# Kernel tuning notes

Measured on AMD Instinct MI355X. Metric: run time of the kernel, lower is better.

Reference implementation:

```python
import jax, jax.numpy as jnp
import numpy as np

NEG_SLOPE = 0.2

def setup_inputs() -> dict:
    key = jax.random.key(0)
    k1, k2, k3, k4 = jax.random.split(key, 4)
    B, n, d_in, d_out = 8, 2048, 128, 128
    x = jax.random.normal(k1, (B, n, d_in), dtype=jnp.float32)
    adj = jax.random.uniform(k2, (B, n, n), dtype=jnp.float32)
    # glorot init for W: std = sqrt(2/(fan_in+fan_out))
    W = jax.random.normal(k3, (d_in, d_out), dtype=jnp.float32) * np.sqrt(2.0 / (d_in + d_out))
    a = jax.random.normal(k4, (2 * d_out,), dtype=jnp.float32) * np.sqrt(2.0 / (2 * d_out + 1))
    return {"x": x, "adj": adj, "W": W, "a": a}

def reference(x, adj, W, a):
    d_out = W.shape[1]
    h = jnp.einsum('bni,io->bno', x, W)               # [B,n,d_out]
    x_weighted = jnp.einsum('bnm,bmo->bno', adj, h)   # adj @ Wx
    # additive attention: a @ concat(h_i, h_j) == h_i@a_src + h_j@a_dst
    a_src, a_dst = a[:d_out], a[d_out:]
    s_i = h @ a_src                                   # [B,n]
    s_j = h @ a_dst                                   # [B,n]
    e = jax.nn.leaky_relu(s_i[:, :, None] + s_j[:, None, :], NEG_SLOPE)  # [B,n,n]
    alpha = jax.nn.softmax(e, axis=2)
    out = jnp.einsum('bnm,bmo->bno', alpha, h) + x_weighted
    return jax.nn.leaky_relu(out, NEG_SLOPE)
```

## Files before the change

### kernel.cpp

```cpp
#include <hip/hip_runtime.h>
#include <hip/hip_bf16.h>

#define NEG 0.2f
#define LOG2E 1.4426950408889634f

typedef __attribute__((ext_vector_type(8))) short bf16x8;
typedef __attribute__((ext_vector_type(4))) float f32x4;
typedef __attribute__((ext_vector_type(4))) int int4v;

__device__ __forceinline__ float lrelu(float t){ return fmaxf(t, NEG * t); }
__device__ __forceinline__ float fast_exp2(float x){
  float r; asm("v_exp_f32 %0, %1" : "=v"(r) : "v"(x)); return r;
}
__device__ __forceinline__ unsigned short f2bf(float f){
  union { float f; unsigned int u; } v; v.f = f;
  unsigned int r = v.u + 0x7FFFu + ((v.u >> 16) & 1u);
  return (unsigned short)(r >> 16);
}

__global__ __launch_bounds__(256) void k0_wt(const float* __restrict__ W,
                                             unsigned short* __restrict__ Wt){
  __shared__ __align__(16) unsigned short wl[128*136];
  const int t = threadIdx.x;
  {
    const int k = t >> 1, oh = (t & 1) * 64;
#pragma unroll 8
    for (int e = 0; e < 64; ++e)
      wl[(oh + e)*136 + k] = f2bf(W[k*128 + oh + e]);
  }
  __syncthreads();
  {
    const int o = t >> 1, ks = (t & 1) * 64;
#pragma unroll
    for (int g = 0; g < 8; ++g){
      int4v v = *(const int4v*)(wl + o*136 + ks + g*8);
      *(int4v*)(Wt + o*128 + ks + g*8) = v;
    }
  }
}

__global__ __launch_bounds__(256) void k1_fused(const float* __restrict__ x,
                                                const unsigned short* __restrict__ Wt,
                                                const float* __restrict__ a,
                                                unsigned short* __restrict__ ht,
                                                float* __restrict__ ssrcL,
                                                float* __restrict__ sdstL){
  __shared__ __align__(16) unsigned short wtl[128*136];
  __shared__ __align__(16) unsigned short xl[32*136];
  __shared__ __align__(16) unsigned short tlw[128*34];
  __shared__ float sred[2][4][2][16];
  const int t = threadIdx.x;
  const int bx = blockIdx.x;
  const int b  = bx >> 6;
  const int jt = bx & 63;
  const long rowbase = (long)bx * 32;
  {
    const int o = t >> 1, seg = (t & 1) * 64;
    const int4v* src = (const int4v*)(Wt + o*128 + seg);
    int4v* dst = (int4v*)(wtl + o*136 + seg);
#pragma unroll
    for (int g = 0; g < 8; ++g) dst[g] = src[g];
  }
  {
    const int i = t >> 3, ks = (t & 7) * 16;
    const f32x4* src = (const f32x4*)(x + (rowbase + i)*128 + ks);
    unsigned int q[8];
#pragma unroll
    for (int g = 0; g < 4; ++g){
      f32x4 v = src[g];
      q[g*2]   = (unsigned)f2bf(v[0]) | ((unsigned)f2bf(v[1]) << 16);
      q[g*2+1] = (unsigned)f2bf(v[2]) | ((unsigned)f2bf(v[3]) << 16);
    }
    int4v* dst = (int4v*)(xl + i*136 + ks);
    dst[0] = *(int4v*)&q[0];
    dst[1] = *(int4v*)&q[4];
  }
  __syncthreads();
  const int w = t >> 6, lane = t & 63, lr = lane & 15, hi = lane >> 4;
  f32x4 zro = {0.f, 0.f, 0.f, 0.f};
  f32x4 acc00 = zro, acc01 = zro, acc10 = zro, acc11 = zro;
#pragma unroll
  for (int ks = 0; ks < 4; ++ks){
    const bf16x8 a0 = *(const bf16x8*)(wtl + (w*32      + lr)*136 + ks*32 + hi*8);
    const bf16x8 a1 = *(const bf16x8*)(wtl + (w*32 + 16 + lr)*136 + ks*32 + hi*8);
    const bf16x8 b0 = *(const bf16x8*)(xl + (     lr)*136 + ks*32 + hi*8);
    const bf16x8 b1 = *(const bf16x8*)(xl + (16 + lr)*136 + ks*32 + hi*8);
    acc00 = __builtin_amdgcn_mfma_f32_16x16x32_bf16(a0, b0, acc00, 0, 0, 0);
    acc01 = __builtin_amdgcn_mfma_f32_16x16x32_bf16(a0, b1, acc01, 0, 0, 0);
    acc10 = __builtin_amdgcn_mfma_f32_16x16x32_bf16(a1, b0, acc10, 0, 0, 0);
    acc11 = __builtin_amdgcn_mfma_f32_16x16x32_bf16(a1, b1, acc11, 0, 0, 0);
  }
  {
    const f32x4 as0 = *(const f32x4*)(a +       w*32      + hi*4);
    const f32x4 as1 = *(const f32x4*)(a +       w*32 + 16 + hi*4);
    const f32x4 ad0 = *(const f32x4*)(a + 128 + w*32      + hi*4);
    const f32x4 ad1 = *(const f32x4*)(a + 128 + w*32 + 16 + hi*4);
    float ps0, ps1, pd0, pd1;
    {
      f32x4 u = acc00*as0 + acc10*as1;  ps0 = u[0]+u[1]+u[2]+u[3];
      f32x4 v = acc01*as0 + acc11*as1;  ps1 = v[0]+v[1]+v[2]+v[3];
      f32x4 p = acc00*ad0 + acc10*ad1;  pd0 = p[0]+p[1]+p[2]+p[3];
      f32x4 r = acc01*ad0 + acc11*ad1;  pd1 = r[0]+r[1]+r[2]+r[3];
    }
#pragma unroll
    for (int off = 16; off <= 32; off <<= 1){
      ps0 += __shfl_xor(ps0, off); ps1 += __shfl_xor(ps1, off);
      pd0 += __shfl_xor(pd0, off); pd1 += __shfl_xor(pd1, off);
    }
    if (hi == 0){
      sred[0][w][0][lr] = ps0; sred[0][w][1][lr] = ps1;
      sred[1][w][0][lr] = pd0; sred[1][w][1][lr] = pd1;
    }
  }
#pragma unroll
  for (int q = 0; q < 4; ++q){
    tlw[(w*32      + hi*4 + q)*34      + lr] = f2bf(acc00[q]);
    tlw[(w*32      + hi*4 + q)*34 + 16 + lr] = f2bf(acc01[q]);
    tlw[(w*32 + 16 + hi*4 + q)*34      + lr] = f2bf(acc10[q]);
    tlw[(w*32 + 16 + hi*4 + q)*34 + 16 + lr] = f2bf(acc11[q]);
  }
  __syncthreads();
  {
    const int o = t >> 1, jseg = (t & 1) * 16;
    const unsigned int* src = (const unsigned int*)(tlw + o*34 + jseg);
    unsigned int p[8];
#pragma unroll
    for (int g = 0; g < 8; ++g) p[g] = src[g];
    unsigned short* dst = ht + (long)b*262144 + (long)o*2048 + jt*32 + jseg;
    ((int4v*)dst)[0] = *(int4v*)&p[0];
    ((int4v*)dst)[1] = *(int4v*)&p[4];
  }
  if (t < 64){
    const int sel = t >> 5, jl = t & 31;
    const int ig = jl >> 4, l2 = jl & 15;
    const float s = sred[sel][0][ig][l2] + sred[sel][1][ig][l2]
                  + sred[sel][2][ig][l2] + sred[sel][3][ig][l2];
    if (sel == 0) ssrcL[rowbase + jl] = s * LOG2E;
    else          sdstL[rowbase + jl] = s * LOG2E;
  }
}

__global__ __launch_bounds__(256) void k2_ml(const float* __restrict__ ssrcL,
                                             const float* __restrict__ sdstL,
                                             float* __restrict__ carr){
  const int lane = threadIdx.x & 63;
  const long row = (long)blockIdx.x * 4 + (threadIdx.x >> 6);
  const int b = (int)(row >> 11);
  const float siL = ssrcL[row];
  const float* sd = sdstL + (long)b*2048;
  float mx = -3.4e38f;
#pragma unroll
  for (int k = 0; k < 8; ++k){
    f32x4 v = *(const f32x4*)(sd + lane*4 + k*256);
    mx = fmaxf(mx, fmaxf(fmaxf(v[0], v[1]), fmaxf(v[2], v[3])));
  }
#pragma unroll
  for (int off = 1; off <= 32; off <<= 1) mx = fmaxf(mx, __shfl_xor(mx, off));
  const float mL = lrelu(siL + mx);
  float sum = 0.f;
#pragma unroll
  for (int k = 0; k < 8; ++k){
    f32x4 v = *(const f32x4*)(sd + lane*4 + k*256);
#pragma unroll
    for (int e = 0; e < 4; ++e) sum += fast_exp2(lrelu(siL + v[e]) - mL);
  }
#pragma unroll
  for (int off = 1; off <= 32; off <<= 1) sum += __shfl_xor(sum, off);
  if (lane == 0) carr[row] = mL + __log2f(sum);
}

__global__ __launch_bounds__(256, 2) void k3_main(const float* __restrict__ adj,
                                                  const unsigned short* __restrict__ ht,
                                                  const float* __restrict__ ssrcL,
                                                  const float* __restrict__ sdstL,
                                                  const float* __restrict__ carr,
                                                  float* __restrict__ out){
  __shared__ __align__(16) char smem[40960];
  unsigned short* tl = (unsigned short*)smem;
  float* red = (float*)smem;
  const int t   = threadIdx.x;
  const int bxr = blockIdx.x;
  const int bx  = ((bxr & 7) << 6) | (bxr >> 3);
  const int b   = bx >> 6;
  const int i0  = (bx & 63) * 32;
  const int lane = t & 63;
  const int lr  = lane & 15, hi = lane >> 4;
  const int kh  = t >> 7, wr = (t >> 6) & 1;
  const int rowi = i0 + wr*16 + lr;
  const long rowg = (long)b*2048 + rowi;
  const float siL = ssrcL[rowg];
  const float Ci  = carr[rowg];
  const float* adjrow = adj + rowg*2048 + kh*1024 + hi*8;
  const float* sdb    = sdstL + (long)b*2048 + kh*1024 + hi*8;
  const unsigned short* htg = ht + (long)b*262144;
  const int so = t >> 2, sseg = t & 3;
  const unsigned short* sgp0 = htg + (long)so*2048 + sseg*8;
  const unsigned short* sgp1 = htg + (long)(so + 64)*2048 + sseg*8;
  const int woff0 = so*40 + sseg*8;
  const int woff1 = (so + 64)*40 + sseg*8;

  f32x4 zro = {0.f, 0.f, 0.f, 0.f};
  f32x4 acc[8];
#pragma unroll
  for (int i = 0; i < 8; ++i) acc[i] = zro;

  *(int4v*)(tl + 0*5120 + woff0) = *(const int4v*)(sgp0);
  *(int4v*)(tl + 1*5120 + woff0) = *(const int4v*)(sgp0 + 1024);
  *(int4v*)(tl + 0*5120 + woff1) = *(const int4v*)(sgp1);
  *(int4v*)(tl + 1*5120 + woff1) = *(const int4v*)(sgp1 + 1024);
  int4v hA0 = *(const int4v*)(sgp0 + 32);
  int4v hA1 = *(const int4v*)(sgp0 + 1024 + 32);
  int4v hA2 = *(const int4v*)(sgp1 + 32);
  int4v hA3 = *(const int4v*)(sgp1 + 1024 + 32);
  int4v hB0 = *(const int4v*)(sgp0 + 64);
  int4v hB1 = *(const int4v*)(sgp0 + 1024 + 64);
  int4v hB2 = *(const int4v*)(sgp1 + 64);
  int4v hB3 = *(const int4v*)(sgp1 + 1024 + 64);
  f32x4 aA0 = *(const f32x4*)(adjrow);        f32x4 aA1 = *(const f32x4*)(adjrow + 4);
  f32x4 dA0 = *(const f32x4*)(sdb);           f32x4 dA1 = *(const f32x4*)(sdb + 4);
  f32x4 aB0 = *(const f32x4*)(adjrow + 32);   f32x4 aB1 = *(const f32x4*)(adjrow + 36);
  f32x4 dB0 = *(const f32x4*)(sdb + 32);      f32x4 dB1 = *(const f32x4*)(sdb + 36);
  f32x4 aC0 = *(const f32x4*)(adjrow + 64);   f32x4 aC1 = *(const f32x4*)(adjrow + 68);
  f32x4 dC0 = *(const f32x4*)(sdb + 64);      f32x4 dC1 = *(const f32x4*)(sdb + 68);
  f32x4 aD0 = *(const f32x4*)(adjrow + 96);   f32x4 aD1 = *(const f32x4*)(adjrow + 100);
  f32x4 dD0 = *(const f32x4*)(sdb + 96);      f32x4 dD1 = *(const f32x4*)(sdb + 100);
  asm volatile("s_waitcnt lgkmcnt(0)" ::: "memory");
  __builtin_amdgcn_s_barrier();
  __builtin_amdgcn_sched_barrier(0);

#define K3_ITER(KT, P0, P1, P2, P3, A0, A1, D0, D1, BW, BR)  do{                 \
    *(int4v*)(tl + ((BW)*2+0)*5120 + woff0) = P0;         \
    *(int4v*)(tl + ((BW)*2+1)*5120 + woff0) = P1;                                \
    *(int4v*)(tl + ((BW)*2+0)*5120 + woff1) = P2;                                \
    *(int4v*)(tl + ((BW)*2+1)*5120 + woff1) = P3;                                \
    {  const int j3 = ((KT)+3 < 32 ? (KT)+3 : 31)*32;          \
       P0 = *(const int4v*)(sgp0 + j3);                                          \
       P1 = *(const int4v*)(sgp0 + 1024 + j3);                                   \
       P2 = *(const int4v*)(sgp1 + j3);                                          \
       P3 = *(const int4v*)(sgp1 + 1024 + j3); }                                 \
    bf16x8 af;                                                                   \
    {  float w[8];                                                               \
       _Pragma("unroll")                                                         \
       for (int e = 0; e < 4; ++e){                                              \
         const float u0 = siL + D0[e];                                           \
         w[e]     = A0[e] + fast_exp2(lrelu(u0) - Ci);                           \
         const float u1 = siL + D1[e];                                           \
         w[4 + e] = A1[e] + fast_exp2(lrelu(u1) - Ci);                           \
       }                                                                         \
       const unsigned int p01 = __builtin_amdgcn_perm(__float_as_uint(w[1]), __float_as_uint(w[0]), 0x07060302u); \
       const unsigned int p23 = __builtin_amdgcn_perm(__float_as_uint(w[3]), __float_as_uint(w[2]), 0x07060302u); \
       const unsigned int p45 = __builtin_amdgcn_perm(__float_as_uint(w[5]), __float_as_uint(w[4]), 0x07060302u); \
       const unsigned int p67 = __builtin_amdgcn_perm(__float_as_uint(w[7]), __float_as_uint(w[6]), 0x07060302u); \
       int4v ai = {(int)p01, (int)p23, (int)p45, (int)p67};                      \
       af = *(bf16x8*)&ai;                                                       \
    }                                                                            \
    {  const int j4 = ((KT)+4 < 32 ? (KT)+4 : 31)*32;      \
       A0 = *(const f32x4*)(adjrow + j4);                                        \
       A1 = *(const f32x4*)(adjrow + j4 + 4);                                    \
       D0 = *(const f32x4*)(sdb + j4);                                           \
       D1 = *(const f32x4*)(sdb + j4 + 4); }                                     \
    __builtin_amdgcn_s_setprio(1);                                               \
    _Pragma("unroll")                                                            \
    for (int cg = 0; cg < 8; ++cg){                                              \
      const bf16x8 bfv = *(const bf16x8*)(tl + ((BR)*2+kh)*5120 + (cg*16 + lr)*40 + hi*8); \
      acc[cg] = __builtin_amdgcn_mfma_f32_16x16x32_bf16(af, bfv, acc[cg], 0, 0, 0); \
    }                                                                            \
    __builtin_amdgcn_s_setprio(0);                                               \
    asm volatile("s_waitcnt lgkmcnt(0)" ::: "memory");                           \
    __builtin_amdgcn_s_barrier();                                                \
    __builtin_amdgcn_sched_barrier(0);                                           \
  }while(0)

  for (int kt = 0; kt < 32; kt += 4){
    K3_ITER(kt,     hA0, hA1, hA2, hA3, aA0, aA1, dA0, dA1, 1, 0);
    K3_ITER(kt + 1, hB0, hB1, hB2, hB3, aB0, aB1, dB0, dB1, 0, 1);
    K3_ITER(kt + 2, hA0, hA1, hA2, hA3, aC0, aC1, dC0, dC1, 1, 0);
    K3_ITER(kt + 3, hB0, hB1, hB2, hB3, aD0, aD1, dD0, dD1, 0, 1);
  }
#undef K3_ITER

  if (kh == 1){
#pragma unroll
    for (int cg = 0; cg < 8; ++cg)
#pragma unroll
      for (int q = 0; q < 4; ++q)
        red[(wr*16 + hi*4 + q)*128 + cg*16 + lr] = acc[cg][q];
  }
  __syncthreads();
  if (kh == 0){
#pragma unroll
    for (int cg = 0; cg < 8; ++cg){
#pragma unroll
      for (int q = 0; q < 4; ++q){
        const int rl2 = wr*16 + hi*4 + q;
        const float v = acc[cg][q] + red[rl2*128 + cg*16 + lr];
        out[((long)b*2048 + i0 + rl2)*128 + cg*16 + lr] = lrelu(v);
      }
    }
  }
}

extern "C" void kernel_launch(void* const* d_in, const int* in_sizes, int n_in,
                              void* d_out, int out_size, void* d_ws, size_t ws_size,
                              hipStream_t stream){
  const float* x   = (const float*)d_in[0];
  const float* adj = (const float*)d_in[1];
  const float* W   = (const float*)d_in[2];
  const float* a   = (const float*)d_in[3];
  float* out = (float*)d_out;
  char* ws = (char*)d_ws;

  unsigned short* ht    = (unsigned short*)(ws);
  float*          ssrcL = (float*)(ws + 4194304);
  float*          sdstL = (float*)(ws + 4259840);
  float*          carr  = (float*)(ws + 4325376);
  unsigned short* Wt    = (unsigned short*)(ws + 4390912);

  k0_wt   <<<1,    256, 0, stream>>>(W, Wt);
  k1_fused<<<512,  256, 0, stream>>>(x, Wt, a, ht, ssrcL, sdstL);
  k2_ml   <<<4096, 256, 0, stream>>>(ssrcL, sdstL, carr);
  k3_main <<<512,  256, 0, stream>>>(adj, ht, ssrcL, sdstL, carr, out);
}
```

Measured before the change: 63.18 us.

## Restructure main kernel around 32x32 MFMA with direct global-to-LDS staging

Rewrites the main attention-aggregation kernel to use 2 waves per block, each owning half of the K dimension and running 32x32x16 bf16 MFMAs. The h tiles are staged with global_load_lds into a double-buffered, XOR-swizzled LDS layout. This removes the register round trip and the per-step block barriers, which are replaced by vmcnt waits. Adj and score vectors are prefetched two stages ahead. The trade-offs are 64 KB of LDS per block and half the threads per block, which may reduce occupancy and latency hiding.

```diff
diff --git a/kernel.cpp b/kernel.cpp
--- a/kernel.cpp
+++ b/kernel.cpp
@@ -6,6 +6,7 @@
 
 typedef __attribute__((ext_vector_type(8))) short bf16x8;
 typedef __attribute__((ext_vector_type(4))) float f32x4;
+typedef __attribute__((ext_vector_type(16))) float f32x16;
 typedef __attribute__((ext_vector_type(4))) int int4v;
 
 __device__ __forceinline__ float lrelu(float t){ return fmaxf(t, NEG * t); }
@@ -169,134 +170,121 @@
   if (lane == 0) carr[row] = mL + __log2f(sum);
 }
 
-__global__ __launch_bounds__(256, 2) void k3_main(const float* __restrict__ adj,
-                                                  const unsigned short* __restrict__ ht,
-                                                  const float* __restrict__ ssrcL,
-                                                  const float* __restrict__ sdstL,
-                                                  const float* __restrict__ carr,
-                                                  float* __restrict__ out){
-  __shared__ __align__(16) char smem[40960];
-  unsigned short* tl = (unsigned short*)smem;
+__global__ __launch_bounds__(128) void k3_main(const float* __restrict__ adj,
+                                               const unsigned short* __restrict__ ht,
+                                               const float* __restrict__ ssrcL,
+                                               const float* __restrict__ sdstL,
+                                               const float* __restrict__ carr,
+                                               float* __restrict__ out){
+  __shared__ __align__(16) char smem[65536];
+  unsigned short (*tl)[2][128][64] = (unsigned short (*)[2][128][64])smem;
   float* red = (float*)smem;
   const int t   = threadIdx.x;
   const int bxr = blockIdx.x;
   const int bx  = ((bxr & 7) << 6) | (bxr >> 3);
   const int b   = bx >> 6;
   const int i0  = (bx & 63) * 32;
-  const int lane = t & 63;
-  const int lr  = lane & 15, hi = lane >> 4;
-  const int kh  = t >> 7, wr = (t >> 6) & 1;
-  const int rowi = i0 + wr*16 + lr;
-  const long rowg = (long)b*2048 + rowi;
+  const int w   = t >> 6, lane = t & 63;
+  const int r32 = lane & 31, ks = lane >> 5;
+  const long rowg = (long)b*2048 + i0 + r32;
   const float siL = ssrcL[rowg];
   const float Ci  = carr[rowg];
-  const float* adjrow = adj + rowg*2048 + kh*1024 + hi*8;
-  const float* sdb    = sdstL + (long)b*2048 + kh*1024 + hi*8;
-  const unsigned short* htg = ht + (long)b*262144;
-  const int so = t >> 2, sseg = t & 3;
-  const unsigned short* sgp0 = htg + (long)so*2048 + sseg*8;
-  const unsigned short* sgp1 = htg + (long)(so + 64)*2048 + sseg*8;
-  const int woff0 = so*40 + sseg*8;
-  const int woff1 = (so + 64)*40 + sseg*8;
-
-  f32x4 zro = {0.f, 0.f, 0.f, 0.f};
-  f32x4 acc[8];
-#pragma unroll
-  for (int i = 0; i < 8; ++i) acc[i] = zro;
-
-  *(int4v*)(tl + 0*5120 + woff0) = *(const int4v*)(sgp0);
-  *(int4v*)(tl + 1*5120 + woff0) = *(const int4v*)(sgp0 + 1024);
-  *(int4v*)(tl + 0*5120 + woff1) = *(const int4v*)(sgp1);
-  *(int4v*)(tl + 1*5120 + woff1) = *(const int4v*)(sgp1 + 1024);
-  int4v hA0 = *(const int4v*)(sgp0 + 32);
-  int4v hA1 = *(const int4v*)(sgp0 + 1024 + 32);
-  int4v hA2 = *(const int4v*)(sgp1 + 32);
-  int4v hA3 = *(const int4v*)(sgp1 + 1024 + 32);
-  int4v hB0 = *(const int4v*)(sgp0 + 64);
-  int4v hB1 = *(const int4v*)(sgp0 + 1024 + 64);
-  int4v hB2 = *(const int4v*)(sgp1 + 64);
-  int4v hB3 = *(const int4v*)(sgp1 + 1024 + 64);
-  f32x4 aA0 = *(const f32x4*)(adjrow);        f32x4 aA1 = *(const f32x4*)(adjrow + 4);
-  f32x4 dA0 = *(const f32x4*)(sdb);           f32x4 dA1 = *(const f32x4*)(sdb + 4);
-  f32x4 aB0 = *(const f32x4*)(adjrow + 32);   f32x4 aB1 = *(const f32x4*)(adjrow + 36);
-  f32x4 dB0 = *(const f32x4*)(sdb + 32);      f32x4 dB1 = *(const f32x4*)(sdb + 36);
-  f32x4 aC0 = *(const f32x4*)(adjrow + 64);   f32x4 aC1 = *(const f32x4*)(adjrow + 68);
-  f32x4 dC0 = *(const f32x4*)(sdb + 64);      f32x4 dC1 = *(const f32x4*)(sdb + 68);
-  f32x4 aD0 = *(const f32x4*)(adjrow + 96);   f32x4 aD1 = *(const f32x4*)(adjrow + 100);
-  f32x4 dD0 = *(const f32x4*)(sdb + 96);      f32x4 dD1 = *(const f32x4*)(sdb + 100);
-  asm volatile("s_waitcnt lgkmcnt(0)" ::: "memory");
-  __builtin_amdgcn_s_barrier();
-  __builtin_amdgcn_sched_barrier(0);
-
-#define K3_ITER(KT, P0, P1, P2, P3, A0, A1, D0, D1, BW, BR)  do{                 \
-    *(int4v*)(tl + ((BW)*2+0)*5120 + woff0) = P0;         \
-    *(int4v*)(tl + ((BW)*2+1)*5120 + woff0) = P1;                                \
-    *(int4v*)(tl + ((BW)*2+0)*5120 + woff1) = P2;                                \
-    *(int4v*)(tl + ((BW)*2+1)*5120 + woff1) = P3;                                \
-    {  const int j3 = ((KT)+3 < 32 ? (KT)+3 : 31)*32;          \
-       P0 = *(const int4v*)(sgp0 + j3);                                          \
-       P1 = *(const int4v*)(sgp0 + 1024 + j3);                                   \
-       P2 = *(const int4v*)(sgp1 + j3);                                          \
-       P3 = *(const int4v*)(sgp1 + 1024 + j3); }                                 \
-    bf16x8 af;                                                                   \
-    {  float w[8];                                                               \
-       _Pragma("unroll")                                                         \
-       for (int e = 0; e < 4; ++e){                                              \
-         const float u0 = siL + D0[e];                                           \
-         w[e]     = A0[e] + fast_exp2(lrelu(u0) - Ci);                           \
-         const float u1 = siL + D1[e];                                           \
-         w[4 + e] = A1[e] + fast_exp2(lrelu(u1) - Ci);                           \
-       }                                                                         \
-       const unsigned int p01 = __builtin_amdgcn_perm(__float_as_uint(w[1]), __float_as_uint(w[0]), 0x07060302u); \
-       const unsigned int p23 = __builtin_amdgcn_perm(__float_as_uint(w[3]), __float_as_uint(w[2]), 0x07060302u); \
-       const unsigned int p45 = __builtin_amdgcn_perm(__float_as_uint(w[5]), __float_as_uint(w[4]), 0x07060302u); \
-       const unsigned int p67 = __builtin_amdgcn_perm(__float_as_uint(w[7]), __float_as_uint(w[6]), 0x07060302u); \
-       int4v ai = {(int)p01, (int)p23, (int)p45, (int)p67};                      \
-       af = *(bf16x8*)&ai;                                                       \
+  const float* adjrow = adj + rowg*2048 + w*1024;
+  const float* sdb    = sdstL + (long)b*2048 + w*1024;
+  const unsigned short* sgbase = ht + (long)b*262144 + w*1024
+                               + ((lane & 7) ^ ((lane >> 3) & 7)) * 8
+                               + (long)(lane >> 3) * 2048;
+
+#define K3_STAGE(BB, JB) do{                                                     \
+    _Pragma("unroll")                                                            \
+    for (int ii = 0; ii < 16; ++ii){                                             \
+      __builtin_amdgcn_global_load_lds(                                          \
+        (const __attribute__((address_space(1))) void*)(sgbase + (JB) + ii*16384),\
+        (__attribute__((address_space(3))) void*)&tl[BB][w][ii*8][0], 16, 0, 0); \
     }                                                                            \
-    {  const int j4 = ((KT)+4 < 32 ? (KT)+4 : 31)*32;      \
-       A0 = *(const f32x4*)(adjrow + j4);                                        \
-       A1 = *(const f32x4*)(adjrow + j4 + 4);                                    \
-       D0 = *(const f32x4*)(sdb + j4);                                           \
-       D1 = *(const f32x4*)(sdb + j4 + 4); }                                     \
-    __builtin_amdgcn_s_setprio(1);                                               \
-    _Pragma("unroll")                                                            \
-    for (int cg = 0; cg < 8; ++cg){                                              \
-      const bf16x8 bfv = *(const bf16x8*)(tl + ((BR)*2+kh)*5120 + (cg*16 + lr)*40 + hi*8); \
-      acc[cg] = __builtin_amdgcn_mfma_f32_16x16x32_bf16(af, bfv, acc[cg], 0, 0, 0); \
-    }                                                                            \
-    __builtin_amdgcn_s_setprio(0);                                               \
-    asm volatile("s_waitcnt lgkmcnt(0)" ::: "memory");                           \
-    __builtin_amdgcn_s_barrier();                                                \
     __builtin_amdgcn_sched_barrier(0);                                           \
   }while(0)
 
-  for (int kt = 0; kt < 32; kt += 4){
-    K3_ITER(kt,     hA0, hA1, hA2, hA3, aA0, aA1, dA0, dA1, 1, 0);
-    K3_ITER(kt + 1, hB0, hB1, hB2, hB3, aB0, aB1, dB0, dB1, 0, 1);
-    K3_ITER(kt + 2, hA0, hA1, hA2, hA3, aC0, aC1, dC0, dC1, 1, 0);
-    K3_ITER(kt + 3, hB0, hB1, hB2, hB3, aD0, aD1, dD0, dD1, 0, 1);
-  }
-#undef K3_ITER
-
-  if (kh == 1){
-#pragma unroll
-    for (int cg = 0; cg < 8; ++cg)
-#pragma unroll
-      for (int q = 0; q < 4; ++q)
-        red[(wr*16 + hi*4 + q)*128 + cg*16 + lr] = acc[cg][q];
-  }
-  __syncthreads();
-  if (kh == 0){
-#pragma unroll
-    for (int cg = 0; cg < 8; ++cg){
-#pragma unroll
-      for (int q = 0; q < 4; ++q){
-        const int rl2 = wr*16 + hi*4 + q;
-        const float v = acc[cg][q] + red[rl2*128 + cg*16 + lr];
-        out[((long)b*2048 + i0 + rl2)*128 + cg*16 + lr] = lrelu(v);
+#define K3_LOADSET(SL, JB) do{                                                   \
+    _Pragma("unroll")                                                            \
+    for (int g = 0; g < 4; ++g){                                                 \
+      av[SL][g*2]   = *(const f32x4*)(adjrow + (JB) + g*16 + ks*8);              \
+      av[SL][g*2+1] = *(const f32x4*)(adjrow + (JB) + g*16 + ks*8 + 4);          \
+      dv[SL][g*2]   = *(const f32x4*)(sdb    + (JB) + g*16 + ks*8);              \
+      dv[SL][g*2+1] = *(const f32x4*)(sdb    + (JB) + g*16 + ks*8 + 4);          \
+    }                                                                            \
+  }while(0)
+
+  f32x4 av[2][8], dv[2][8];
+  f32x16 acc[4];
+#pragma unroll
+  for (int f = 0; f < 4; ++f)
+#pragma unroll
+    for (int e = 0; e < 16; ++e) acc[f][e] = 0.f;
+
+  K3_STAGE(0, 0);
+  K3_LOADSET(0, 0);
+  K3_LOADSET(1, 64);
+  asm volatile("s_waitcnt vmcnt(32)" ::: "memory");
+  __builtin_amdgcn_sched_barrier(0);
+
+#pragma unroll
+  for (int i = 0; i < 16; ++i){
+    const int cur = i & 1;
+    if (i < 15) K3_STAGE(cur ^ 1, (i + 1) * 64);
+    bf16x8 af[4];
+#pragma unroll
+    for (int g = 0; g < 4; ++g){
+      float wv[8];
+#pragma unroll
+      for (int e = 0; e < 4; ++e){
+        wv[e]     = av[cur][g*2][e]   + fast_exp2(lrelu(siL + dv[cur][g*2][e])   - Ci);
+        wv[4 + e] = av[cur][g*2+1][e] + fast_exp2(lrelu(siL + dv[cur][g*2+1][e]) - Ci);
       }
-    }
+      const unsigned int p01 = __builtin_amdgcn_perm(__float_as_uint(wv[1]), __float_as_uint(wv[0]), 0x07060302u);
+      const unsigned int p23 = __builtin_amdgcn_perm(__float_as_uint(wv[3]), __float_as_uint(wv[2]), 0x07060302u);
+      const unsigned int p45 = __builtin_amdgcn_perm(__float_as_uint(wv[5]), __float_as_uint(wv[4]), 0x07060302u);
+      const unsigned int p67 = __builtin_amdgcn_perm(__float_as_uint(wv[7]), __float_as_uint(wv[6]), 0x07060302u);
+      int4v ai = {(int)p01, (int)p23, (int)p45, (int)p67};
+      af[g] = *(bf16x8*)&ai;
+    }
+    if (i < 14) K3_LOADSET(cur, (i + 2) * 64);
+#pragma unroll
+    for (int g = 0; g < 4; ++g){
+      const int cph = ((g*2 + ks) ^ (lane & 7)) * 8;
+#pragma unroll
+      for (int f = 0; f < 4; ++f){
+        const bf16x8 bf = *(const bf16x8*)&tl[cur][w][f*32 + r32][cph];
+        acc[f] = __builtin_amdgcn_mfma_f32_32x32x16_bf16(af[g], bf, acc[f], 0, 0, 0);
+      }
+    }
+    if (i < 14)      asm volatile("s_waitcnt vmcnt(16)" ::: "memory");
+    else if (i == 14) asm volatile("s_waitcnt vmcnt(0)"  ::: "memory");
+    __builtin_amdgcn_sched_barrier(0);
+  }
+#undef K3_STAGE
+#undef K3_LOADSET
+
+  __syncthreads();
+  if (w == 1){
+#pragma unroll
+    for (int f = 0; f < 4; ++f)
+#pragma unroll
+      for (int rg = 0; rg < 16; ++rg){
+        const int rr = (rg & 3) + 8*(rg >> 2) + 4*ks;
+        red[rr*128 + f*32 + r32] = acc[f][rg];
+      }
+  }
+  __syncthreads();
+  if (w == 0){
+#pragma unroll
+    for (int f = 0; f < 4; ++f)
+#pragma unroll
+      for (int rg = 0; rg < 16; ++rg){
+        const int rr = (rg & 3) + 8*(rg >> 2) + 4*ks;
+        const float v = acc[f][rg] + red[rr*128 + f*32 + r32];
+        out[((long)b*2048 + i0 + rr)*128 + f*32 + r32] = lrelu(v);
+      }
   }
 }
 
@@ -319,5 +307,5 @@
   k0_wt   <<<1,    256, 0, stream>>>(W, Wt);
   k1_fused<<<512,  256, 0, stream>>>(x, Wt, a, ht, ssrcL, sdstL);
   k2_ml   <<<4096, 256, 0, stream>>>(ssrcL, sdstL, carr);
-  k3_main <<<512,  256, 0, stream>>>(adj, ht, ssrcL, sdstL, carr, out);
-}
+  k3_main <<<512,  128, 0, stream>>>(adj, ht, ssrcL, sdstL, carr, out);
+}
```

Result: slower. 64.55 us (+2.2%).
